# Kernel optimization log

Hardware: AMD Instinct MI355X
Metric: run time of the kernel (lower is better)

Reference implementation:

```python
import jax, jax.numpy as jnp
import numpy as np
import math

F_DIM = 256      # feature_dims
NHEADS = 4
KEY_D = 64
VAL_D = 64
ITERS = 6        # update_iters
N_ATOMS = 100000
N_BONDS = 200000
NEI = 6
ATOM_FDIM = 31
BOND_FDIM = 37   # 31 + 6
NEG_SLOPE = 0.1


def setup_inputs() -> dict:
    key = jax.random.key(0)
    ks = jax.random.split(key, 13)
    s = 0.05
    return {
        "fatoms": jax.random.normal(ks[0], (N_ATOMS, ATOM_FDIM), jnp.float32),
        "fbonds": jax.random.normal(ks[1], (N_BONDS, BOND_FDIM), jnp.float32),
        "agraph": jax.random.randint(ks[2], (N_ATOMS, NEI), 0, N_BONDS),
        "bgraph": jax.random.randint(ks[3], (N_BONDS, NEI), 0, N_BONDS),
        "lig_scope": jax.random.randint(ks[4], (64, 2), 0, N_ATOMS),
        "W_emb": jax.random.normal(ks[5], (BOND_FDIM, F_DIM), jnp.float32) * s,
        "b_emb": jnp.zeros((F_DIM,), jnp.float32),
        "Wq": jax.random.normal(ks[6], (F_DIM, NHEADS * KEY_D), jnp.float32) * s,
        "Wk": jax.random.normal(ks[7], (F_DIM, NHEADS * KEY_D), jnp.float32) * s,
        "Wv": jax.random.normal(ks[8], (F_DIM, NHEADS * VAL_D), jnp.float32) * s,
        "Wout": jax.random.normal(ks[9], (VAL_D, F_DIM), jnp.float32) * s,
        "W_last": jax.random.normal(ks[10], (ATOM_FDIM + F_DIM, F_DIM), jnp.float32) * s,
        "b_last": jnp.zeros((F_DIM,), jnp.float32),
    }


def reference(fatoms, fbonds, agraph, bgraph, lig_scope,
              W_emb, b_emb, Wq, Wk, Wv, Wout, W_last, b_last):
    # Bond embedding + initial message
    fbonds_input = fbonds @ W_emb + b_emb                      # [B, F]
    message = jax.nn.leaky_relu(fbonds_input, NEG_SLOPE)
    # index 0 is the padding bond -> masked out in attention
    nei_mask = jnp.where(bgraph != 0, 0.0, -1e7)[:, None, :]   # [B, 1, NEI]
    inv_sqrt_kd = 1.0 / math.sqrt(KEY_D)

    for _ in range(ITERS - 1):
        nei = message[bgraph]                                  # [B, NEI, F] gather
        q = (message @ Wq).reshape(N_BONDS, NHEADS, KEY_D)     # [B, H, K]
        k = (nei @ Wk).reshape(N_BONDS, NEI, NHEADS, KEY_D)    # [B, NEI, H, K]
        v = (nei @ Wv).reshape(N_BONDS, NEI, NHEADS, VAL_D)    # [B, NEI, H, V]
        scores = jnp.einsum('bhk,bnhk->bhn', q, k) * inv_sqrt_kd + nei_mask
        attn = jax.nn.softmax(scores, axis=-1)                 # [B, H, NEI]
        out = jnp.einsum('bhn,bnhv->bhv', attn, v)             # [B, H, V]
        out = out.mean(axis=1)                                 # mean over heads -> [B, V]
        message = jax.nn.leaky_relu(fbonds_input + out @ Wout, NEG_SLOPE)

    # Aggregate incoming bond messages per atom (index 0 acts as padding row)
    nei_sum = message[agraph].sum(axis=1)                      # [A, F]
    h = jnp.concatenate([fatoms, nei_sum], axis=-1) @ W_last + b_last
    return jax.nn.leaky_relu(h, NEG_SLOPE)
```

## Files before the change

kernel.cpp:

```cpp
#include <hip/hip_runtime.h>

#define N_ATOMS 100000
#define N_BONDS 200000
#define NEI 6
#define ITERS 6

#define MB_PAD 200064
#define MT_B 1563
#define MT_A 782
#define KL 320
#define KVSTRIDE 768

typedef __bf16 bf16x8 __attribute__((ext_vector_type(8)));
typedef float f32x4 __attribute__((ext_vector_type(4)));

__device__ __forceinline__ float b2f(unsigned short u) {
  union { unsigned int i; float f; } x; x.i = ((unsigned int)u) << 16; return x.f;
}
__device__ __forceinline__ unsigned short f2b(float f) {
  union { float f; unsigned int i; } x; x.f = f;
  unsigned int r = (x.i + 0x7FFFu + ((x.i >> 16) & 1u)) >> 16;
  return (unsigned short)r;
}
__device__ __forceinline__ float lrelu(float v) { return v > 0.f ? v : 0.1f * v; }

#if defined(__has_builtin)
#  if __has_builtin(__builtin_amdgcn_cvt_f32_fp8) && __has_builtin(__builtin_amdgcn_cvt_pk_fp8_f32)
#    define HW_FP8 1
#  endif
#endif

__device__ __forceinline__ unsigned char f2e4m3_sw(float f) {
  union { float f; unsigned u; } x; x.f = f;
  unsigned s = (x.u >> 24) & 0x80u;
  unsigned ax = x.u & 0x7FFFFFFFu;
  if (ax >= 0x43E00000u) return (unsigned char)(s | 0x7Eu);
  if (ax < 0x3A800000u)  return (unsigned char)s;
  if (ax < 0x3C800000u) {
    union { unsigned u; float f; } a; a.u = ax;
    unsigned n = (unsigned)(a.f * 512.0f + 0.5f);
    return (unsigned char)(s | n);
  }
  unsigned r = ax + 0x0007FFFFu + ((ax >> 20) & 1u);
  unsigned e32 = r >> 23;
  unsigned mant = (r >> 20) & 7u;
  int e8 = (int)e32 - 120;
  if (e8 >= 16) return (unsigned char)(s | 0x7Eu);
  return (unsigned char)(s | ((unsigned)e8 << 3) | mant);
}
__device__ __forceinline__ float dec8_sw(unsigned b) {
  unsigned s = (b & 0x80u) << 24;
  unsigned e = (b >> 3) & 0xFu, m = b & 7u;
  if (e) { union { unsigned u; float f; } x; x.u = s | ((e + 120u) << 23) | (m << 20); return x.f; }
  float v = (float)m * 0.001953125f;
  return (b & 0x80u) ? -v : v;
}
#ifdef HW_FP8
__device__ __forceinline__ unsigned char f2e4m3(float f) {
  return (unsigned char)(__builtin_amdgcn_cvt_pk_fp8_f32(f, f, 0, false) & 0xFF);
}
#define DEC0(x) __builtin_amdgcn_cvt_f32_fp8((int)(x), 0)
#define DEC1(x) __builtin_amdgcn_cvt_f32_fp8((int)(x), 1)
#define DEC2(x) __builtin_amdgcn_cvt_f32_fp8((int)(x), 2)
#define DEC3(x) __builtin_amdgcn_cvt_f32_fp8((int)(x), 3)
#else
__device__ __forceinline__ unsigned char f2e4m3(float f) { return f2e4m3_sw(f); }
#define DEC0(x) dec8_sw((x) & 0xFFu)
#define DEC1(x) dec8_sw(((x) >> 8) & 0xFFu)
#define DEC2(x) dec8_sw(((x) >> 16) & 0xFFu)
#define DEC3(x) dec8_sw(((x) >> 24) & 0xFFu)
#endif

__global__ __launch_bounds__(256) void pack_weights(
    const float* __restrict__ Wq, const float* __restrict__ Wk,
    const float* __restrict__ Wv, const float* __restrict__ Wemb,
    const float* __restrict__ Wout, const float* __restrict__ Wlast,
    unsigned short* __restrict__ wkvT, unsigned short* __restrict__ wqT,
    unsigned short* __restrict__ wmsgT, unsigned short* __restrict__ wlastT)
{
  int t = blockIdx.x * 256 + threadIdx.x;
  {
    int n = t >> 8, k = t & 255;
    wkvT[t] = f2b((n < 256) ? Wk[k * 256 + n] : Wv[k * 256 + (n - 256)]);
  }
  if (t < 65536) {
    int n = t >> 8, k = t & 255;
    wqT[t] = f2b(Wq[k * 256 + n]);
  }
  if (t < 32768) {
    int n = t >> 7, k = t & 127;
    float v = 0.f;
    if (k < 64)       v = Wout[k * 256 + n];
    else if (k < 101) v = Wemb[(k - 64) * 256 + n];
    wmsgT[t] = f2b(v);
  }
  if (t < 256 * KL) {
    int n = t / KL, k = t % KL;
    float v = 0.f;
    if (k < 256)      v = Wlast[(31 + k) * 256 + n];
    else if (k < 287) v = Wlast[(k - 256) * 256 + n];
    wlastT[t] = f2b(v);
  }
}

__global__ __launch_bounds__(256) void pack_bonds(
    const float* __restrict__ fbonds, unsigned short* __restrict__ A2)
{
  int t = blockIdx.x * 256 + threadIdx.x;
  int r = t >> 7, c = t & 127;
  float v = 0.f;
  if (c >= 64 && c < 101 && r < N_BONDS) v = fbonds[r * 37 + (c - 64)];
  A2[t] = f2b(v);
}

template<int EP>
__global__ __launch_bounds__(256) void gemm_bt(
    const unsigned short* __restrict__ A,
    const unsigned short* __restrict__ BT,
    unsigned short* __restrict__ C0,
    float* __restrict__ Fout,
    const float* __restrict__ Xf,
    int K, int N, int Mreal)
{
  __shared__ __align__(16) unsigned short As[128 * 64];
  __shared__ __align__(16) unsigned short Bs[128 * 64];
  const int tid  = threadIdx.x;
  const int wave = tid >> 6, lane = tid & 63;
  const int wr = wave >> 1, wc = wave & 1;
  const int lhi = lane >> 4, llo = lane & 15;
  const int mBase = blockIdx.x * 128;
  const int nBase = blockIdx.y * 128;
  const int crow = tid >> 3, ccol = tid & 7;

  f32x4 acc[4][4];
  #pragma unroll
  for (int i = 0; i < 4; ++i)
    #pragma unroll
    for (int j = 0; j < 4; ++j)
      acc[i][j] = f32x4{0.f, 0.f, 0.f, 0.f};

  for (int k0 = 0; k0 < K; k0 += 64) {
    __syncthreads();
    #pragma unroll
    for (int r = 0; r < 4; ++r) {
      const unsigned short* ga =
          A + (size_t)(mBase + r * 32 + crow) * K + (k0 + ccol * 8);
      __builtin_amdgcn_global_load_lds(
          (const __attribute__((address_space(1))) void*)ga,
          (__attribute__((address_space(3))) void*)(As + r * 2048 + wave * 512), 16, 0, 0);
      const unsigned short* gb =
          BT + (size_t)(nBase + r * 32 + crow) * K + (k0 + ccol * 8);
      __builtin_amdgcn_global_load_lds(
          (const __attribute__((address_space(1))) void*)gb,
          (__attribute__((address_space(3))) void*)(Bs + r * 2048 + wave * 512), 16, 0, 0);
    }
    __syncthreads();
    #pragma unroll
    for (int ks = 0; ks < 2; ++ks) {
      bf16x8 af[4], bfv[4];
      #pragma unroll
      for (int i = 0; i < 4; ++i)
        af[i] = *reinterpret_cast<const bf16x8*>(&As[(wr * 64 + i * 16 + llo) * 64 + ks * 32 + lhi * 8]);
      #pragma unroll
      for (int j = 0; j < 4; ++j)
        bfv[j] = *reinterpret_cast<const bf16x8*>(&Bs[(wc * 64 + j * 16 + llo) * 64 + ks * 32 + lhi * 8]);
      #pragma unroll
      for (int i = 0; i < 4; ++i)
        #pragma unroll
        for (int j = 0; j < 4; ++j)
          acc[i][j] = __builtin_amdgcn_mfma_f32_16x16x32_bf16(af[i], bfv[j], acc[i][j], 0, 0, 0);
    }
  }

  #pragma unroll
  for (int i = 0; i < 4; ++i) {
    #pragma unroll
    for (int j = 0; j < 4; ++j) {
      const int col = nBase + wc * 64 + j * 16 + llo;
      #pragma unroll
      for (int r = 0; r < 4; ++r) {
        const int row = mBase + wr * 64 + i * 16 + lhi * 4 + r;
        const float v = acc[i][j][r];
        if (EP == 0) {
          C0[(size_t)row * N + col] = f2b(v);
        } else if (EP == 1) {
          C0[(size_t)row * N + col] = f2b(lrelu(v + Xf[col]));
        } else if (EP == 3) {
          if (row < Mreal) Fout[(size_t)row * N + col] = lrelu(v + Xf[col]);
        } else {
          unsigned char* kvb = (unsigned char*)C0;
          if (nBase < 256) {
            kvb[(size_t)row * KVSTRIDE + col] = f2e4m3(v);
          } else {
            *(unsigned short*)(kvb + (size_t)row * KVSTRIDE + 256 +
                               (size_t)(col - 256) * 2) = f2b(v);
          }
        }
      }
    }
  }
}

__global__ __launch_bounds__(256) void attn_merged(
    const unsigned short* __restrict__ q,
    const unsigned char* __restrict__ kv,
    const int* __restrict__ bgraph,
    unsigned short* __restrict__ A2,
    int rowOff)
{
  const int wid  = rowOff + blockIdx.x * 4 + (threadIdx.x >> 6);
  const int lane = threadIdx.x & 63;
  if (wid >= N_BONDS) return;

  const ushort4 qu = *reinterpret_cast<const ushort4*>(
      q + (size_t)(wid - rowOff) * 256 + lane * 4);
  const float q0 = b2f(qu.x), q1 = b2f(qu.y), q2 = b2f(qu.z), q3 = b2f(qu.w);

  int bn[NEI];
  #pragma unroll
  for (int n = 0; n < NEI; ++n) bn[n] = bgraph[wid * NEI + n];

  unsigned kdw[NEI]; ushort4 vu[NEI];
  #pragma unroll
  for (int n = 0; n < NEI; ++n) {
    const unsigned char* base = kv + (size_t)bn[n] * KVSTRIDE;
    kdw[n] = *reinterpret_cast<const unsigned*>(base + lane * 4);
    vu[n]  = *reinterpret_cast<const ushort4*>(base + 256 + lane * 8);
  }

  float sc[NEI];
  #pragma unroll
  for (int n = 0; n < NEI; ++n) {
    float p = q0 * DEC0(kdw[n]) + q1 * DEC1(kdw[n]) +
              q2 * DEC2(kdw[n]) + q3 * DEC3(kdw[n]);
    p += __shfl_xor(p, 1); p += __shfl_xor(p, 2);
    p += __shfl_xor(p, 4); p += __shfl_xor(p, 8);
    sc[n] = p * 0.125f + (bn[n] != 0 ? 0.f : -1e7f);
  }
  float m = sc[0];
  #pragma unroll
  for (int n = 1; n < NEI; ++n) m = fmaxf(m, sc[n]);
  float e[NEI], s = 0.f;
  #pragma unroll
  for (int n = 0; n < NEI; ++n) { e[n] = __expf(sc[n] - m); s += e[n]; }
  const float inv = 1.f / s;

  float o0 = 0, o1 = 0, o2 = 0, o3 = 0;
  #pragma unroll
  for (int n = 0; n < NEI; ++n) {
    const float a = e[n] * inv;
    o0 += a * b2f(vu[n].x); o1 += a * b2f(vu[n].y);
    o2 += a * b2f(vu[n].z); o3 += a * b2f(vu[n].w);
  }
  o0 += __shfl_xor(o0, 16); o0 += __shfl_xor(o0, 32);
  o1 += __shfl_xor(o1, 16); o1 += __shfl_xor(o1, 32);
  o2 += __shfl_xor(o2, 16); o2 += __shfl_xor(o2, 32);
  o3 += __shfl_xor(o3, 16); o3 += __shfl_xor(o3, 32);
  if (lane < 16) {
    ushort4 ov;
    ov.x = f2b(o0 * 0.25f); ov.y = f2b(o1 * 0.25f);
    ov.z = f2b(o2 * 0.25f); ov.w = f2b(o3 * 0.25f);
    *reinterpret_cast<ushort4*>(A2 + (size_t)wid * 128 + lane * 4) = ov;
  }
}

__global__ __launch_bounds__(256) void atom_gather(
    const unsigned short* __restrict__ msg,
    const int* __restrict__ agraph,
    const float* __restrict__ fatoms,
    unsigned short* __restrict__ apad)
{
  const int aid  = blockIdx.x * 4 + (threadIdx.x >> 6);
  const int lane = threadIdx.x & 63;
  if (aid >= N_ATOMS) return;
  float s0 = 0, s1 = 0, s2 = 0, s3 = 0;
  #pragma unroll
  for (int n = 0; n < NEI; ++n) {
    const int b = agraph[aid * NEI + n];
    const ushort4 u = *reinterpret_cast<const ushort4*>(msg + (size_t)b * 256 + lane * 4);
    s0 += b2f(u.x); s1 += b2f(u.y); s2 += b2f(u.z); s3 += b2f(u.w);
  }
  ushort4 ov; ov.x = f2b(s0); ov.y = f2b(s1); ov.z = f2b(s2); ov.w = f2b(s3);
  *reinterpret_cast<ushort4*>(apad + (size_t)aid * KL + lane * 4) = ov;
  apad[(size_t)aid * KL + 256 + lane] =
      (lane < 31) ? f2b(fatoms[(size_t)aid * 31 + lane]) : (unsigned short)0;
}

__global__ __launch_bounds__(256) void diag_out(float* out, int n, float code) {
  int t = blockIdx.x * 256 + threadIdx.x;
  if (t < n) out[t] = (t == 0) ? code : 0.f;
}

extern "C" void kernel_launch(void* const* d_in, const int* in_sizes, int n_in,
                              void* d_out, int out_size, void* d_ws, size_t ws_size,
                              hipStream_t stream) {
  const float* fatoms = (const float*)d_in[0];
  const float* fbonds = (const float*)d_in[1];
  const int* agraph   = (const int*)d_in[2];
  const int* bgraph   = (const int*)d_in[3];
  const float* Wemb   = (const float*)d_in[5];
  const float* bemb   = (const float*)d_in[6];
  const float* Wq     = (const float*)d_in[7];
  const float* Wk     = (const float*)d_in[8];
  const float* Wv     = (const float*)d_in[9];
  const float* Wout   = (const float*)d_in[10];
  const float* Wlast  = (const float*)d_in[11];
  const float* blast  = (const float*)d_in[12];
  float* out          = (float*)d_out;

  char* ws = (char*)d_ws;
  size_t off = 0;
  auto alloc = [&](size_t bytes) {
    char* p = ws + off; off += (bytes + 511) & ~(size_t)511; return p;
  };
  unsigned short* msg    = (unsigned short*)alloc((size_t)MB_PAD * 256 * 2);
  unsigned char*  kv     = (unsigned char*)alloc((size_t)MB_PAD * KVSTRIDE);
  unsigned short* A2     = (unsigned short*)alloc((size_t)MB_PAD * 128 * 2);
  unsigned short* wkvT   = (unsigned short*)alloc((size_t)512 * 256 * 2);
  unsigned short* wqT    = (unsigned short*)alloc((size_t)256 * 256 * 2);
  unsigned short* wmsgT  = (unsigned short*)alloc((size_t)256 * 128 * 2);
  unsigned short* wlastT = (unsigned short*)alloc((size_t)256 * KL * 2);
  unsigned short* apad   = (unsigned short*)kv;

  long long remain = (long long)ws_size - (long long)off;
  int qrows = 0;
  if (remain >= 128 * 512) {
    long long r = remain / 512;
    if (r > MB_PAD) r = MB_PAD;
    qrows = (int)(r & ~127LL);
  }
  unsigned short* q = (unsigned short*)(ws + off);

  if (qrows < 128) {
    diag_out<<<dim3((out_size + 255) / 256), dim3(256), 0, stream>>>(
        out, out_size, 10000.f + (float)(ws_size >> 20));
    return;
  }

  pack_weights<<<dim3(512), dim3(256), 0, stream>>>(
      Wq, Wk, Wv, Wemb, Wout, Wlast, wkvT, wqT, wmsgT, wlastT);
  pack_bonds<<<dim3(MB_PAD * 128 / 256), dim3(256), 0, stream>>>(fbonds, A2);

  gemm_bt<1><<<dim3(MT_B, 2), dim3(256), 0, stream>>>(
      A2, wmsgT, msg, (float*)nullptr, bemb, 128, 256, MB_PAD);

  for (int it = 0; it < ITERS - 1; ++it) {
    int rows0 = MB_PAD < qrows ? MB_PAD : qrows;
    gemm_bt<0><<<dim3(rows0 / 128, 2), dim3(256), 0, stream>>>(
        msg, wqT, q, (float*)nullptr, (const float*)nullptr, 256, 256, MB_PAD);
    gemm_bt<4><<<dim3(MT_B, 4), dim3(256), 0, stream>>>(
        msg, wkvT, (unsigned short*)kv, (float*)nullptr, (const float*)nullptr,
        256, 512, MB_PAD);
    attn_merged<<<dim3(rows0 / 4), dim3(256), 0, stream>>>(q, kv, bgraph, A2, 0);
    for (int rowOff = qrows; rowOff < N_BONDS; rowOff += qrows) {
      int rows = MB_PAD - rowOff; if (rows > qrows) rows = qrows;
      gemm_bt<0><<<dim3(rows / 128, 2), dim3(256), 0, stream>>>(
          msg + (size_t)rowOff * 256, wqT, q, (float*)nullptr,
          (const float*)nullptr, 256, 256, MB_PAD);
      attn_merged<<<dim3(rows / 4), dim3(256), 0, stream>>>(
          q, kv, bgraph, A2, rowOff);
    }
    gemm_bt<1><<<dim3(MT_B, 2), dim3(256), 0, stream>>>(
        A2, wmsgT, msg, (float*)nullptr, bemb, 128, 256, MB_PAD);
  }

  atom_gather<<<dim3(N_ATOMS / 4), dim3(256), 0, stream>>>(msg, agraph, fatoms, apad);
  gemm_bt<3><<<dim3(MT_A, 2), dim3(256), 0, stream>>>(
      apad, wlastT, (unsigned short*)nullptr, out, blast, KL, 256, N_ATOMS);
}
```

Measured before the change: 2.254 ms.

## Fuse Q projection GEMM into attention kernel, keeping Q tile in LDS

Replaces the separate Q GEMM plus attention launches with one kernel per 128-bond tile. The kernel computes Q via MFMA into shared memory, then runs the neighbour softmax-attention with software-pipelined double-buffered gathers of K/V. This removes the global round trip of the Q buffer, the chunked launch loop and the need for workspace for Q. It also folds the softmax scale into exp2 and uses a hardware reciprocal. In exchange it needs a large LDS footprint (about 66KB per block), which may limit occupancy, and the reciprocal is approximate.

```diff
diff --git a/kernel.cpp b/kernel.cpp
--- a/kernel.cpp
+++ b/kernel.cpp
@@ -10,6 +10,7 @@
 #define MT_A 782
 #define KL 320
 #define KVSTRIDE 768
+#define QSTR 260
 
 typedef __bf16 bf16x8 __attribute__((ext_vector_type(8)));
 typedef float f32x4 __attribute__((ext_vector_type(4)));
@@ -201,66 +202,151 @@
   }
 }
 
-__global__ __launch_bounds__(256) void attn_merged(
-    const unsigned short* __restrict__ q,
+#define LOADSET(bn_, kd_, vu_, BL) do {                                        \
+    const int wid_ = mBase + (BL);                                             \
+    _Pragma("unroll")                                                          \
+    for (int n = 0; n < NEI; ++n) bn_[n] = bgraph[(size_t)wid_ * NEI + n];     \
+    _Pragma("unroll")                                                          \
+    for (int n = 0; n < NEI; ++n) {                                            \
+      const unsigned char* bp_ = kv + (size_t)bn_[n] * KVSTRIDE;               \
+      kd_[n] = *reinterpret_cast<const unsigned*>(bp_ + lane * 4);             \
+      vu_[n] = *reinterpret_cast<const ushort4*>(bp_ + 256 + lane * 8);        \
+    }                                                                          \
+  } while (0)
+
+#define COMPUTEB(bn_, kd_, vu_, BL) do {                                       \
+    const int wid_ = mBase + (BL);                                             \
+    const ushort4 qu_ = *reinterpret_cast<const ushort4*>(                     \
+        &smem[(size_t)(BL) * QSTR + lane * 4]);                                \
+    const float q0_ = b2f(qu_.x), q1_ = b2f(qu_.y);                            \
+    const float q2_ = b2f(qu_.z), q3_ = b2f(qu_.w);                            \
+    float sc_[NEI];                                                            \
+    _Pragma("unroll")                                                          \
+    for (int n = 0; n < NEI; ++n) {                                            \
+      float p_ = q0_ * DEC0(kd_[n]) + q1_ * DEC1(kd_[n]) +                     \
+                 q2_ * DEC2(kd_[n]) + q3_ * DEC3(kd_[n]);                      \
+      p_ += __shfl_xor(p_, 1); p_ += __shfl_xor(p_, 2);                        \
+      p_ += __shfl_xor(p_, 4); p_ += __shfl_xor(p_, 8);                        \
+      sc_[n] = p_ * SCL + (bn_[n] != 0 ? 0.f : -1e7f);                         \
+    }                                                                          \
+    const float m_ =                                                           \
+        fmaxf(fmaxf(fmaxf(sc_[0], sc_[1]), fmaxf(sc_[2], sc_[3])),             \
+              fmaxf(sc_[4], sc_[5]));                                          \
+    float s_ = 0.f, o0_ = 0.f, o1_ = 0.f, o2_ = 0.f, o3_ = 0.f;                \
+    _Pragma("unroll")                                                          \
+    for (int n = 0; n < NEI; ++n) {                                            \
+      const float e_ = exp2f(sc_[n] - m_);                                     \
+      s_ += e_;                                                                \
+      o0_ += e_ * b2f(vu_[n].x); o1_ += e_ * b2f(vu_[n].y);                    \
+      o2_ += e_ * b2f(vu_[n].z); o3_ += e_ * b2f(vu_[n].w);                    \
+    }                                                                          \
+    const float inv_ = 0.25f * __builtin_amdgcn_rcpf(s_);                      \
+    o0_ *= inv_; o1_ *= inv_; o2_ *= inv_; o3_ *= inv_;                        \
+    o0_ += __shfl_xor(o0_, 16); o0_ += __shfl_xor(o0_, 32);                    \
+    o1_ += __shfl_xor(o1_, 16); o1_ += __shfl_xor(o1_, 32);                    \
+    o2_ += __shfl_xor(o2_, 16); o2_ += __shfl_xor(o2_, 32);                    \
+    o3_ += __shfl_xor(o3_, 16); o3_ += __shfl_xor(o3_, 32);                    \
+    if (lane < 16) {                                                           \
+      ushort4 ov_;                                                             \
+      ov_.x = f2b(o0_); ov_.y = f2b(o1_);                                      \
+      ov_.z = f2b(o2_); ov_.w = f2b(o3_);                                      \
+      *reinterpret_cast<ushort4*>(A2 + (size_t)wid_ * 128 + lane * 4) = ov_;   \
+    }                                                                          \
+  } while (0)
+
+__global__ __launch_bounds__(512, 4) void fused_qattn(
+    const unsigned short* __restrict__ msg,
+    const unsigned short* __restrict__ wqT,
     const unsigned char* __restrict__ kv,
     const int* __restrict__ bgraph,
-    unsigned short* __restrict__ A2,
-    int rowOff)
+    unsigned short* __restrict__ A2)
 {
-  const int wid  = rowOff + blockIdx.x * 4 + (threadIdx.x >> 6);
-  const int lane = threadIdx.x & 63;
-  if (wid >= N_BONDS) return;
-
-  const ushort4 qu = *reinterpret_cast<const ushort4*>(
-      q + (size_t)(wid - rowOff) * 256 + lane * 4);
-  const float q0 = b2f(qu.x), q1 = b2f(qu.y), q2 = b2f(qu.z), q3 = b2f(qu.w);
-
-  int bn[NEI];
+  __shared__ __align__(16) unsigned short smem[128 * QSTR];
+  const int tid  = threadIdx.x;
+  const int wave = tid >> 6, lane = tid & 63;
+  const int wr = wave >> 2, wc = wave & 3;
+  const int lhi = lane >> 4, llo = lane & 15;
+  const int mBase = blockIdx.x * 128;
+  const int crow = tid >> 3, ccol = tid & 7;
+
+  f32x4 acc[4][4];
   #pragma unroll
-  for (int n = 0; n < NEI; ++n) bn[n] = bgraph[wid * NEI + n];
-
-  unsigned kdw[NEI]; ushort4 vu[NEI];
+  for (int i = 0; i < 4; ++i)
+    #pragma unroll
+    for (int j = 0; j < 4; ++j)
+      acc[i][j] = f32x4{0.f, 0.f, 0.f, 0.f};
+
+  for (int k0 = 0; k0 < 256; k0 += 64) {
+    __syncthreads();
+    #pragma unroll
+    for (int r = 0; r < 2; ++r) {
+      const unsigned short* ga =
+          msg + (size_t)(mBase + r * 64 + crow) * 256 + (k0 + ccol * 8);
+      __builtin_amdgcn_global_load_lds(
+          (const __attribute__((address_space(1))) void*)ga,
+          (__attribute__((address_space(3))) void*)(smem + r * 4096 + wave * 512),
+          16, 0, 0);
+    }
+    #pragma unroll
+    for (int r = 0; r < 4; ++r) {
+      const unsigned short* gb =
+          wqT + (size_t)(r * 64 + crow) * 256 + (k0 + ccol * 8);
+      __builtin_amdgcn_global_load_lds(
+          (const __attribute__((address_space(1))) void*)gb,
+          (__attribute__((address_space(3))) void*)(smem + 8192 + r * 4096 + wave * 512),
+          16, 0, 0);
+    }
+    __syncthreads();
+    #pragma unroll
+    for (int ks = 0; ks < 2; ++ks) {
+      bf16x8 af[4], bfv[4];
+      #pragma unroll
+      for (int i = 0; i < 4; ++i)
+        af[i] = *reinterpret_cast<const bf16x8*>(
+            &smem[(wr * 64 + i * 16 + llo) * 64 + ks * 32 + lhi * 8]);
+      #pragma unroll
+      for (int j = 0; j < 4; ++j)
+        bfv[j] = *reinterpret_cast<const bf16x8*>(
+            &smem[8192 + (wc * 64 + j * 16 + llo) * 64 + ks * 32 + lhi * 8]);
+      #pragma unroll
+      for (int i = 0; i < 4; ++i)
+        #pragma unroll
+        for (int j = 0; j < 4; ++j)
+          acc[i][j] = __builtin_amdgcn_mfma_f32_16x16x32_bf16(af[i], bfv[j], acc[i][j], 0, 0, 0);
+    }
+  }
+  __syncthreads();
+
   #pragma unroll
-  for (int n = 0; n < NEI; ++n) {
-    const unsigned char* base = kv + (size_t)bn[n] * KVSTRIDE;
-    kdw[n] = *reinterpret_cast<const unsigned*>(base + lane * 4);
-    vu[n]  = *reinterpret_cast<const ushort4*>(base + 256 + lane * 8);
-  }
-
-  float sc[NEI];
-  #pragma unroll
-  for (int n = 0; n < NEI; ++n) {
-    float p = q0 * DEC0(kdw[n]) + q1 * DEC1(kdw[n]) +
-              q2 * DEC2(kdw[n]) + q3 * DEC3(kdw[n]);
-    p += __shfl_xor(p, 1); p += __shfl_xor(p, 2);
-    p += __shfl_xor(p, 4); p += __shfl_xor(p, 8);
-    sc[n] = p * 0.125f + (bn[n] != 0 ? 0.f : -1e7f);
-  }
-  float m = sc[0];
-  #pragma unroll
-  for (int n = 1; n < NEI; ++n) m = fmaxf(m, sc[n]);
-  float e[NEI], s = 0.f;
-  #pragma unroll
-  for (int n = 0; n < NEI; ++n) { e[n] = __expf(sc[n] - m); s += e[n]; }
-  const float inv = 1.f / s;
-
-  float o0 = 0, o1 = 0, o2 = 0, o3 = 0;
-  #pragma unroll
-  for (int n = 0; n < NEI; ++n) {
-    const float a = e[n] * inv;
-    o0 += a * b2f(vu[n].x); o1 += a * b2f(vu[n].y);
-    o2 += a * b2f(vu[n].z); o3 += a * b2f(vu[n].w);
-  }
-  o0 += __shfl_xor(o0, 16); o0 += __shfl_xor(o0, 32);
-  o1 += __shfl_xor(o1, 16); o1 += __shfl_xor(o1, 32);
-  o2 += __shfl_xor(o2, 16); o2 += __shfl_xor(o2, 32);
-  o3 += __shfl_xor(o3, 16); o3 += __shfl_xor(o3, 32);
-  if (lane < 16) {
-    ushort4 ov;
-    ov.x = f2b(o0 * 0.25f); ov.y = f2b(o1 * 0.25f);
-    ov.z = f2b(o2 * 0.25f); ov.w = f2b(o3 * 0.25f);
-    *reinterpret_cast<ushort4*>(A2 + (size_t)wid * 128 + lane * 4) = ov;
+  for (int i = 0; i < 4; ++i) {
+    #pragma unroll
+    for (int j = 0; j < 4; ++j) {
+      const int col = wc * 64 + j * 16 + llo;
+      #pragma unroll
+      for (int r = 0; r < 4; ++r) {
+        const int row = wr * 64 + i * 16 + lhi * 4 + r;
+        smem[row * QSTR + col] = f2b(acc[i][j][r]);
+      }
+    }
+  }
+  __syncthreads();
+
+  const float SCL = 0.125f * 1.44269504089f;
+  int bnA[NEI], bnB[NEI];
+  unsigned kdA[NEI], kdB[NEI];
+  ushort4 vuA[NEI], vuB[NEI];
+  const int b0 = wave * 16;
+  int nv = N_BONDS - (mBase + b0);
+  if (nv > 16) nv = 16;
+  if (nv > 0) {
+    LOADSET(bnA, kdA, vuA, b0);
+    #pragma unroll 1
+    for (int it = 0; it < 16; it += 2) {
+      if (it + 1 < nv) LOADSET(bnB, kdB, vuB, b0 + it + 1);
+      if (it < nv)     COMPUTEB(bnA, kdA, vuA, b0 + it);
+      if (it + 2 < nv) LOADSET(bnA, kdA, vuA, b0 + it + 2);
+      if (it + 1 < nv) COMPUTEB(bnB, kdB, vuB, b0 + it + 1);
+    }
   }
 }
 
@@ -322,16 +408,7 @@
   unsigned short* wlastT = (unsigned short*)alloc((size_t)256 * KL * 2);
   unsigned short* apad   = (unsigned short*)kv;
 
-  long long remain = (long long)ws_size - (long long)off;
-  int qrows = 0;
-  if (remain >= 128 * 512) {
-    long long r = remain / 512;
-    if (r > MB_PAD) r = MB_PAD;
-    qrows = (int)(r & ~127LL);
-  }
-  unsigned short* q = (unsigned short*)(ws + off);
-
-  if (qrows < 128) {
+  if (off > ws_size) {
     diag_out<<<dim3((out_size + 255) / 256), dim3(256), 0, stream>>>(
         out, out_size, 10000.f + (float)(ws_size >> 20));
     return;
@@ -345,21 +422,10 @@
       A2, wmsgT, msg, (float*)nullptr, bemb, 128, 256, MB_PAD);
 
   for (int it = 0; it < ITERS - 1; ++it) {
-    int rows0 = MB_PAD < qrows ? MB_PAD : qrows;
-    gemm_bt<0><<<dim3(rows0 / 128, 2), dim3(256), 0, stream>>>(
-        msg, wqT, q, (float*)nullptr, (const float*)nullptr, 256, 256, MB_PAD);
     gemm_bt<4><<<dim3(MT_B, 4), dim3(256), 0, stream>>>(
         msg, wkvT, (unsigned short*)kv, (float*)nullptr, (const float*)nullptr,
         256, 512, MB_PAD);
-    attn_merged<<<dim3(rows0 / 4), dim3(256), 0, stream>>>(q, kv, bgraph, A2, 0);
-    for (int rowOff = qrows; rowOff < N_BONDS; rowOff += qrows) {
-      int rows = MB_PAD - rowOff; if (rows > qrows) rows = qrows;
-      gemm_bt<0><<<dim3(rows / 128, 2), dim3(256), 0, stream>>>(
-          msg + (size_t)rowOff * 256, wqT, q, (float*)nullptr,
-          (const float*)nullptr, 256, 256, MB_PAD);
-      attn_merged<<<dim3(rows / 4), dim3(256), 0, stream>>>(
-          q, kv, bgraph, A2, rowOff);
-    }
+    fused_qattn<<<dim3(MT_B), dim3(512), 0, stream>>>(msg, wqT, kv, bgraph, A2);
     gemm_bt<1><<<dim3(MT_B, 2), dim3(256), 0, stream>>>(
         A2, wmsgT, msg, (float*)nullptr, bemb, 128, 256, MB_PAD);
   }
```

Result: faster. 2.149 ms (-4.7%).

## Fuse Q projection GEMM into attention kernel and swizzle B tiles in LDS

Applied to the files above, without the earlier changes.

Replaces the separate Q GEMM plus attention kernels with one fused kernel. Each 512-thread block computes a 64-row Q tile with MFMA, stages it in shared memory and runs the neighbour attention for those rows. This removes the round trip of q through global memory and the workspace-dependent chunking. Weights are also pre-swizzled along K so the B-tile LDS reads avoid bank conflicts, and softmax switches to exp2 with a folded scale and a fast reciprocal. The cost is that each block reloads the full Wq and the fused kernel's occupancy may limit latency hiding for the gathers.

```diff
diff --git a/kernel.cpp b/kernel.cpp
--- a/kernel.cpp
+++ b/kernel.cpp
@@ -7,9 +7,11 @@
 
 #define MB_PAD 200064
 #define MT_B 1563
+#define MT_Q 3126
 #define MT_A 782
 #define KL 320
 #define KVSTRIDE 768
+#define QSTR 260
 
 typedef __bf16 bf16x8 __attribute__((ext_vector_type(8)));
 typedef float f32x4 __attribute__((ext_vector_type(4)));
@@ -71,6 +73,10 @@
 #define DEC3(x) dec8_sw(((x) >> 24) & 0xFFu)
 #endif
 
+__device__ __forceinline__ int kswz(int k, int n) {
+  return (k & ~63) | ((k & 63) ^ ((n & 7) << 3));
+}
+
 __global__ __launch_bounds__(256) void pack_weights(
     const float* __restrict__ Wq, const float* __restrict__ Wk,
     const float* __restrict__ Wv, const float* __restrict__ Wemb,
@@ -81,25 +87,26 @@
   int t = blockIdx.x * 256 + threadIdx.x;
   {
     int n = t >> 8, k = t & 255;
-    wkvT[t] = f2b((n < 256) ? Wk[k * 256 + n] : Wv[k * 256 + (n - 256)]);
+    wkvT[n * 256 + kswz(k, n)] =
+        f2b((n < 256) ? Wk[k * 256 + n] : Wv[k * 256 + (n - 256)]);
   }
   if (t < 65536) {
     int n = t >> 8, k = t & 255;
-    wqT[t] = f2b(Wq[k * 256 + n]);
+    wqT[n * 256 + kswz(k, n)] = f2b(Wq[k * 256 + n]);
   }
   if (t < 32768) {
     int n = t >> 7, k = t & 127;
     float v = 0.f;
     if (k < 64)       v = Wout[k * 256 + n];
     else if (k < 101) v = Wemb[(k - 64) * 256 + n];
-    wmsgT[t] = f2b(v);
+    wmsgT[n * 128 + kswz(k, n)] = f2b(v);
   }
   if (t < 256 * KL) {
     int n = t / KL, k = t % KL;
     float v = 0.f;
     if (k < 256)      v = Wlast[(31 + k) * 256 + n];
     else if (k < 287) v = Wlast[(k - 256) * 256 + n];
-    wlastT[t] = f2b(v);
+    wlastT[n * KL + kswz(k, n)] = f2b(v);
   }
 }
 
@@ -163,7 +170,8 @@
         af[i] = *reinterpret_cast<const bf16x8*>(&As[(wr * 64 + i * 16 + llo) * 64 + ks * 32 + lhi * 8]);
       #pragma unroll
       for (int j = 0; j < 4; ++j)
-        bfv[j] = *reinterpret_cast<const bf16x8*>(&Bs[(wc * 64 + j * 16 + llo) * 64 + ks * 32 + lhi * 8]);
+        bfv[j] = *reinterpret_cast<const bf16x8*>(
+            &Bs[(wc * 64 + j * 16 + llo) * 64 + ((ks * 32 + lhi * 8) ^ ((llo & 7) << 3))]);
       #pragma unroll
       for (int i = 0; i < 4; ++i)
         #pragma unroll
@@ -201,66 +209,133 @@
   }
 }
 
-__global__ __launch_bounds__(256) void attn_merged(
-    const unsigned short* __restrict__ q,
+__global__ __launch_bounds__(512, 6) void fused_qattn(
+    const unsigned short* __restrict__ msg,
+    const unsigned short* __restrict__ wqT,
     const unsigned char* __restrict__ kv,
     const int* __restrict__ bgraph,
-    unsigned short* __restrict__ A2,
-    int rowOff)
+    unsigned short* __restrict__ A2)
 {
-  const int wid  = rowOff + blockIdx.x * 4 + (threadIdx.x >> 6);
-  const int lane = threadIdx.x & 63;
-  if (wid >= N_BONDS) return;
-
-  const ushort4 qu = *reinterpret_cast<const ushort4*>(
-      q + (size_t)(wid - rowOff) * 256 + lane * 4);
-  const float q0 = b2f(qu.x), q1 = b2f(qu.y), q2 = b2f(qu.z), q3 = b2f(qu.w);
-
-  int bn[NEI];
+  __shared__ __align__(16) unsigned short smem[20480];
+  const int tid  = threadIdx.x;
+  const int wave = tid >> 6, lane = tid & 63;
+  const int wr = wave >> 2, wc = wave & 3;
+  const int lhi = lane >> 4, llo = lane & 15;
+  const int mBase = blockIdx.x * 64;
+  const int crow = tid >> 3, ccol = tid & 7;
+
+  f32x4 acc[2][4];
   #pragma unroll
-  for (int n = 0; n < NEI; ++n) bn[n] = bgraph[wid * NEI + n];
-
-  unsigned kdw[NEI]; ushort4 vu[NEI];
+  for (int i = 0; i < 2; ++i)
+    #pragma unroll
+    for (int j = 0; j < 4; ++j)
+      acc[i][j] = f32x4{0.f, 0.f, 0.f, 0.f};
+
+  for (int k0 = 0; k0 < 256; k0 += 64) {
+    __syncthreads();
+    {
+      const unsigned short* ga =
+          msg + (size_t)(mBase + crow) * 256 + (k0 + ccol * 8);
+      __builtin_amdgcn_global_load_lds(
+          (const __attribute__((address_space(1))) void*)ga,
+          (__attribute__((address_space(3))) void*)(smem + wave * 512), 16, 0, 0);
+    }
+    #pragma unroll
+    for (int r = 0; r < 4; ++r) {
+      const unsigned short* gb =
+          wqT + (size_t)(r * 64 + crow) * 256 + (k0 + ccol * 8);
+      __builtin_amdgcn_global_load_lds(
+          (const __attribute__((address_space(1))) void*)gb,
+          (__attribute__((address_space(3))) void*)(smem + 4096 + r * 4096 + wave * 512),
+          16, 0, 0);
+    }
+    __syncthreads();
+    #pragma unroll
+    for (int ks = 0; ks < 2; ++ks) {
+      bf16x8 af[2], bfv[4];
+      #pragma unroll
+      for (int i = 0; i < 2; ++i)
+        af[i] = *reinterpret_cast<const bf16x8*>(
+            &smem[(wr * 32 + i * 16 + llo) * 64 + ks * 32 + lhi * 8]);
+      #pragma unroll
+      for (int j = 0; j < 4; ++j)
+        bfv[j] = *reinterpret_cast<const bf16x8*>(
+            &smem[4096 + (wc * 64 + j * 16 + llo) * 64 +
+                  ((ks * 32 + lhi * 8) ^ ((llo & 7) << 3))]);
+      #pragma unroll
+      for (int i = 0; i < 2; ++i)
+        #pragma unroll
+        for (int j = 0; j < 4; ++j)
+          acc[i][j] = __builtin_amdgcn_mfma_f32_16x16x32_bf16(af[i], bfv[j], acc[i][j], 0, 0, 0);
+    }
+  }
+  __syncthreads();
+
   #pragma unroll
-  for (int n = 0; n < NEI; ++n) {
-    const unsigned char* base = kv + (size_t)bn[n] * KVSTRIDE;
-    kdw[n] = *reinterpret_cast<const unsigned*>(base + lane * 4);
-    vu[n]  = *reinterpret_cast<const ushort4*>(base + 256 + lane * 8);
-  }
-
-  float sc[NEI];
-  #pragma unroll
-  for (int n = 0; n < NEI; ++n) {
-    float p = q0 * DEC0(kdw[n]) + q1 * DEC1(kdw[n]) +
-              q2 * DEC2(kdw[n]) + q3 * DEC3(kdw[n]);
-    p += __shfl_xor(p, 1); p += __shfl_xor(p, 2);
-    p += __shfl_xor(p, 4); p += __shfl_xor(p, 8);
-    sc[n] = p * 0.125f + (bn[n] != 0 ? 0.f : -1e7f);
-  }
-  float m = sc[0];
-  #pragma unroll
-  for (int n = 1; n < NEI; ++n) m = fmaxf(m, sc[n]);
-  float e[NEI], s = 0.f;
-  #pragma unroll
-  for (int n = 0; n < NEI; ++n) { e[n] = __expf(sc[n] - m); s += e[n]; }
-  const float inv = 1.f / s;
-
-  float o0 = 0, o1 = 0, o2 = 0, o3 = 0;
-  #pragma unroll
-  for (int n = 0; n < NEI; ++n) {
-    const float a = e[n] * inv;
-    o0 += a * b2f(vu[n].x); o1 += a * b2f(vu[n].y);
-    o2 += a * b2f(vu[n].z); o3 += a * b2f(vu[n].w);
-  }
-  o0 += __shfl_xor(o0, 16); o0 += __shfl_xor(o0, 32);
-  o1 += __shfl_xor(o1, 16); o1 += __shfl_xor(o1, 32);
-  o2 += __shfl_xor(o2, 16); o2 += __shfl_xor(o2, 32);
-  o3 += __shfl_xor(o3, 16); o3 += __shfl_xor(o3, 32);
-  if (lane < 16) {
-    ushort4 ov;
-    ov.x = f2b(o0 * 0.25f); ov.y = f2b(o1 * 0.25f);
-    ov.z = f2b(o2 * 0.25f); ov.w = f2b(o3 * 0.25f);
-    *reinterpret_cast<ushort4*>(A2 + (size_t)wid * 128 + lane * 4) = ov;
+  for (int i = 0; i < 2; ++i) {
+    #pragma unroll
+    for (int j = 0; j < 4; ++j) {
+      const int col = wc * 64 + j * 16 + llo;
+      #pragma unroll
+      for (int r = 0; r < 4; ++r) {
+        const int row = wr * 32 + i * 16 + lhi * 4 + r;
+        smem[row * QSTR + col] = f2b(acc[i][j][r]);
+      }
+    }
+  }
+  __syncthreads();
+
+  const float SCL = 0.125f * 1.44269504089f;
+  const int b0 = wave * 8;
+  #pragma unroll 1
+  for (int t2 = 0; t2 < 8; ++t2) {
+    const int bl = b0 + t2;
+    const int wid = mBase + bl;
+    if (wid >= N_BONDS) break;
+
+    int bn[NEI];
+    #pragma unroll
+    for (int n = 0; n < NEI; ++n) bn[n] = bgraph[(size_t)wid * NEI + n];
+    unsigned kdw[NEI]; ushort4 vu[NEI];
+    #pragma unroll
+    for (int n = 0; n < NEI; ++n) {
+      const unsigned char* base = kv + (size_t)bn[n] * KVSTRIDE;
+      kdw[n] = *reinterpret_cast<const unsigned*>(base + lane * 4);
+      vu[n]  = *reinterpret_cast<const ushort4*>(base + 256 + lane * 8);
+    }
+    const ushort4 qu = *reinterpret_cast<const ushort4*>(&smem[bl * QSTR + lane * 4]);
+    const float q0 = b2f(qu.x), q1 = b2f(qu.y), q2 = b2f(qu.z), q3 = b2f(qu.w);
+
+    float sc[NEI];
+    #pragma unroll
+    for (int n = 0; n < NEI; ++n) {
+      float p = q0 * DEC0(kdw[n]) + q1 * DEC1(kdw[n]) +
+                q2 * DEC2(kdw[n]) + q3 * DEC3(kdw[n]);
+      p += __shfl_xor(p, 1); p += __shfl_xor(p, 2);
+      p += __shfl_xor(p, 4); p += __shfl_xor(p, 8);
+      sc[n] = p * SCL + (bn[n] != 0 ? 0.f : -1e7f);
+    }
+    const float m =
+        fmaxf(fmaxf(fmaxf(sc[0], sc[1]), fmaxf(sc[2], sc[3])), fmaxf(sc[4], sc[5]));
+    float s = 0.f, o0 = 0.f, o1 = 0.f, o2 = 0.f, o3 = 0.f;
+    #pragma unroll
+    for (int n = 0; n < NEI; ++n) {
+      const float e = exp2f(sc[n] - m);
+      s += e;
+      o0 += e * b2f(vu[n].x); o1 += e * b2f(vu[n].y);
+      o2 += e * b2f(vu[n].z); o3 += e * b2f(vu[n].w);
+    }
+    const float inv = 0.25f * __builtin_amdgcn_rcpf(s);
+    o0 *= inv; o1 *= inv; o2 *= inv; o3 *= inv;
+    o0 += __shfl_xor(o0, 16); o0 += __shfl_xor(o0, 32);
+    o1 += __shfl_xor(o1, 16); o1 += __shfl_xor(o1, 32);
+    o2 += __shfl_xor(o2, 16); o2 += __shfl_xor(o2, 32);
+    o3 += __shfl_xor(o3, 16); o3 += __shfl_xor(o3, 32);
+    if (lane < 16) {
+      ushort4 ov;
+      ov.x = f2b(o0); ov.y = f2b(o1); ov.z = f2b(o2); ov.w = f2b(o3);
+      *reinterpret_cast<ushort4*>(A2 + (size_t)wid * 128 + lane * 4) = ov;
+    }
   }
 }
 
@@ -322,16 +397,7 @@
   unsigned short* wlastT = (unsigned short*)alloc((size_t)256 * KL * 2);
   unsigned short* apad   = (unsigned short*)kv;
 
-  long long remain = (long long)ws_size - (long long)off;
-  int qrows = 0;
-  if (remain >= 128 * 512) {
-    long long r = remain / 512;
-    if (r > MB_PAD) r = MB_PAD;
-    qrows = (int)(r & ~127LL);
-  }
-  unsigned short* q = (unsigned short*)(ws + off);
-
-  if (qrows < 128) {
+  if (off > ws_size) {
     diag_out<<<dim3((out_size + 255) / 256), dim3(256), 0, stream>>>(
         out, out_size, 10000.f + (float)(ws_size >> 20));
     return;
@@ -345,21 +411,10 @@
       A2, wmsgT, msg, (float*)nullptr, bemb, 128, 256, MB_PAD);
 
   for (int it = 0; it < ITERS - 1; ++it) {
-    int rows0 = MB_PAD < qrows ? MB_PAD : qrows;
-    gemm_bt<0><<<dim3(rows0 / 128, 2), dim3(256), 0, stream>>>(
-        msg, wqT, q, (float*)nullptr, (const float*)nullptr, 256, 256, MB_PAD);
     gemm_bt<4><<<dim3(MT_B, 4), dim3(256), 0, stream>>>(
         msg, wkvT, (unsigned short*)kv, (float*)nullptr, (const float*)nullptr,
         256, 512, MB_PAD);
-    attn_merged<<<dim3(rows0 / 4), dim3(256), 0, stream>>>(q, kv, bgraph, A2, 0);
-    for (int rowOff = qrows; rowOff < N_BONDS; rowOff += qrows) {
-      int rows = MB_PAD - rowOff; if (rows > qrows) rows = qrows;
-      gemm_bt<0><<<dim3(rows / 128, 2), dim3(256), 0, stream>>>(
-          msg + (size_t)rowOff * 256, wqT, q, (float*)nullptr,
-          (const float*)nullptr, 256, 256, MB_PAD);
-      attn_merged<<<dim3(rows / 4), dim3(256), 0, stream>>>(
-          q, kv, bgraph, A2, rowOff);
-    }
+    fused_qattn<<<dim3(MT_Q), dim3(512), 0, stream>>>(msg, wqT, kv, bgraph, A2);
     gemm_bt<1><<<dim3(MT_B, 2), dim3(256), 0, stream>>>(
         A2, wmsgT, msg, (float*)nullptr, bemb, 128, 256, MB_PAD);
   }
```

Result: faster. 1.908 ms (-15.4%).
